# Performance work log

Hardware: AMD Instinct MI355X
Metric: run time of the kernel (lower is better)

The kernel has to match this reference:

```python
import jax, jax.numpy as jnp
import numpy as np

WS = 7          # window size
NH = 12         # num heads
DIM = 384       # embed dim
HD = DIM // NH  # head dim
BW = 2048       # B_ = batch * num_windows
N = WS * WS     # tokens per window


def _relative_position_index(ws):
    coords = np.stack(np.meshgrid(np.arange(ws), np.arange(ws), indexing='ij'))  # [2,ws,ws]
    cf = coords.reshape(2, -1)                      # [2, ws*ws]
    rel = cf[:, :, None] - cf[:, None, :]           # [2, N, N]
    rel = rel.transpose(1, 2, 0).copy()             # [N, N, 2]
    rel[:, :, 0] += ws - 1
    rel[:, :, 1] += ws - 1
    rel[:, :, 0] *= 2 * ws - 1
    return jnp.asarray(rel.sum(-1))                 # [N, N] int


REL_IDX = _relative_position_index(WS)


def setup_inputs() -> dict:
    key = jax.random.key(0)
    ks = jax.random.split(key, 6)
    return {
        'x': jax.random.normal(ks[0], (BW, N, DIM), dtype=jnp.float32),
        'qkv_w': jax.random.normal(ks[1], (3 * DIM, DIM), dtype=jnp.float32) * 0.02,
        'qkv_b': jax.random.normal(ks[2], (3 * DIM,), dtype=jnp.float32) * 0.02,
        'proj_w': jax.random.normal(ks[3], (DIM, DIM), dtype=jnp.float32) * 0.02,
        'proj_b': jax.random.normal(ks[4], (DIM,), dtype=jnp.float32) * 0.02,
        'rel_bias_table': jax.random.normal(ks[5], ((2 * WS - 1) ** 2, NH), dtype=jnp.float32) * 0.02,
    }


def reference(x, qkv_w, qkv_b, proj_w, proj_b, rel_bias_table):
    B_, n, c = x.shape
    scale = HD ** -0.5
    qkv = x @ qkv_w.T + qkv_b                                   # [B_, N, 3*DIM]
    qkv = qkv.reshape(B_, n, 3, NH, HD).transpose(2, 0, 3, 1, 4)  # [3, B_, H, N, HD]
    q, k, v = qkv[0], qkv[1], qkv[2]
    attn = jnp.einsum('bhnd,bhmd->bhnm', q * scale, k)           # [B_, H, N, N]
    bias = rel_bias_table[REL_IDX.reshape(-1)].reshape(n, n, NH)  # gather -> [N, N, H]
    attn = attn + bias.transpose(2, 0, 1)[None]                   # add [1, H, N, N]
    attn = jax.nn.softmax(attn, axis=-1)
    out = jnp.einsum('bhnm,bhmd->bhnd', attn, v)                 # [B_, H, N, HD]
    out = out.transpose(0, 2, 1, 3).reshape(B_, n, c)            # [B_, N, C]
    return out @ proj_w.T + proj_b
```

## Files before the change

### kernel.cpp

```cpp
#include <hip/hip_runtime.h>
#include <hip/hip_bf16.h>

#define NH 12
constexpr float SCALE = 0.17677669529663687f;
constexpr int TOKENS = 100352;

using f32x4  = __attribute__((ext_vector_type(4))) float;
using bf16x8 = __attribute__((ext_vector_type(8))) __bf16;

__device__ inline void gload_lds16(const void* g, void* l) {
  __builtin_amdgcn_global_load_lds(
      (const __attribute__((address_space(1))) void*)g,
      (__attribute__((address_space(3))) void*)l, 16, 0, 0);
}

__global__ __launch_bounds__(256) void wa_prep(
    const float* __restrict__ qkv_w, const float* __restrict__ proj_w,
    const float* __restrict__ tbl,
    __bf16* __restrict__ qkv_w_bf, __bf16* __restrict__ proj_w_bf,
    float* __restrict__ biasTt) {
  int p = blockIdx.x * 256 + threadIdx.x;
  if (p < 442368) { qkv_w_bf[p] = (__bf16)qkv_w[p]; return; }
  p -= 442368;
  if (p < 147456) { proj_w_bf[p] = (__bf16)proj_w[p]; return; }
  p -= 147456;
  if (p >= 49152) return;
  int h = p >> 12, rem = p & 4095, j = rem >> 6, i = rem & 63;
  float v;
  if (j >= 49) v = -1e30f;
  else if (i >= 49) v = 0.0f;
  else {
    int py = i / 7, px = i % 7, qy = j / 7, qx = j % 7;
    v = tbl[((py - qy + 6) * 13 + (px - qx + 6)) * NH + h];
  }
  biasTt[p] = v;
}

__global__ __launch_bounds__(256, 2) void wa_qkv(
    const float* __restrict__ x, const __bf16* __restrict__ wq,
    const float* __restrict__ qkv_b, __bf16* __restrict__ qkv) {
  __shared__ __bf16 As[64 * 384];
  __shared__ __bf16 Bs[2][128 * 64];
  const int t = threadIdx.x, lane = t & 63, wv = t >> 6;
  const int lr = lane & 15, ls = lane >> 4;
  const int mb = blockIdx.x;
  const int wr = wv >> 1, wc = wv & 1;
  #pragma unroll
  for (int i = 0; i < 12; ++i) {
    int p = i * 256 + t;
    int row = p / 48, slot = p - row * 48;
    const float* src = x + (size_t)(mb * 64 + row) * 384 + slot * 8;
    float4 a = *(const float4*)src;
    float4 b = *(const float4*)(src + 4);
    bf16x8 o;
    o[0] = (__bf16)a.x; o[1] = (__bf16)a.y; o[2] = (__bf16)a.z; o[3] = (__bf16)a.w;
    o[4] = (__bf16)b.x; o[5] = (__bf16)b.y; o[6] = (__bf16)b.z; o[7] = (__bf16)b.w;
    int sw = (slot & ~7) | ((slot & 7) ^ (row & 7));
    *(bf16x8*)(As + row * 384 + sw * 8) = o;
  }
  auto stage_b = [&](int st, int bp) {
    int nb = st / 6, kk = st - nb * 6;
    #pragma unroll
    for (int j = 0; j < 4; ++j) {
      int p = wv * 256 + j * 64 + lane;
      int c = p >> 3, sl = p & 7;
      int s = sl ^ (c & 7);
      gload_lds16(wq + (size_t)(nb * 128 + c) * 384 + kk * 64 + s * 8, Bs[bp] + p * 8);
    }
  };
  stage_b(0, 0);
  __syncthreads();
  for (int nb = 0; nb < 9; ++nb) {
    f32x4 acc[2][4] = {};
    for (int kk = 0; kk < 6; ++kk) {
      int st = nb * 6 + kk;
      if (st < 53) stage_b(st + 1, (st + 1) & 1);
      const __bf16* B = Bs[st & 1];
      #pragma unroll
      for (int ks = 0; ks < 2; ++ks) {
        bf16x8 af[2], bfr[4];
        #pragma unroll
        for (int rt = 0; rt < 2; ++rt) {
          int row = wr * 32 + rt * 16 + lr;
          int slot = kk * 8 + ks * 4 + ls;
          int sw = (slot & ~7) | ((slot & 7) ^ (row & 7));
          af[rt] = *(const bf16x8*)(As + row * 384 + sw * 8);
        }
        #pragma unroll
        for (int ct = 0; ct < 4; ++ct) {
          int c = wc * 64 + ct * 16 + lr;
          bfr[ct] = *(const bf16x8*)(B + (c * 8 + ((ks * 4 + ls) ^ (c & 7))) * 8);
        }
        #pragma unroll
        for (int rt = 0; rt < 2; ++rt)
          #pragma unroll
          for (int ct = 0; ct < 4; ++ct)
            acc[rt][ct] = __builtin_amdgcn_mfma_f32_16x16x32_bf16(af[rt], bfr[ct], acc[rt][ct], 0, 0, 0);
      }
      __syncthreads();
    }
    float bias[4];
    #pragma unroll
    for (int ct = 0; ct < 4; ++ct) bias[ct] = qkv_b[nb * 128 + wc * 64 + ct * 16 + lr];
    #pragma unroll
    for (int rt = 0; rt < 2; ++rt)
      #pragma unroll
      for (int r = 0; r < 4; ++r) {
        int row = wr * 32 + rt * 16 + ls * 4 + r;
        __bf16* dst = qkv + (size_t)(mb * 64 + row) * 1152 + nb * 128 + wc * 64;
        #pragma unroll
        for (int ct = 0; ct < 4; ++ct)
          dst[ct * 16 + lr] = (__bf16)(acc[rt][ct][r] + bias[ct]);
      }
  }
}

__global__ __launch_bounds__(256, 3) void wa_attn(
    const float* __restrict__ biasTt, __bf16* __restrict__ qkv) {
  __shared__ __bf16 Pbuf[4][4096];
  __shared__ __bf16 Vbuf[4][2048];
  const int t = threadIdx.x, lane = t & 63, wv = t >> 6;
  const int lr = lane & 15, ls = lane >> 4;
  const int pair = blockIdx.x * 4 + wv;
  const int w = pair / NH, h = pair - w * NH;
  const int w49 = w * 49;
  __bf16* Pw = Pbuf[wv];
  __bf16* Vw = Vbuf[wv];
  f32x4 zero = {0.f, 0.f, 0.f, 0.f};
  bf16x8 ones;
  #pragma unroll
  for (int e = 0; e < 8; ++e) ones[e] = (__bf16)1.0f;

  {
    int row = lane;
    int tok = w49 + (row < 49 ? row : 48);
    const bf16x8* vsrc = (const bf16x8*)(qkv + (size_t)tok * 1152 + 768 + h * 32);
    int f = (row & 3) ^ ((row >> 3) & 3);
    #pragma unroll
    for (int c = 0; c < 4; ++c)
      *(bf16x8*)(Vw + row * 32 + ((c ^ f) * 8)) = vsrc[c];
  }
  bf16x8 qa[4], kb[4];
  #pragma unroll
  for (int rt = 0; rt < 4; ++rt) {
    int tok = min(w49 + rt * 16 + lr, TOKENS - 1);
    qa[rt] = *(const bf16x8*)(qkv + (size_t)tok * 1152 + h * 32 + ls * 8);
  }
  #pragma unroll
  for (int ct = 0; ct < 4; ++ct) {
    int tok = min(w49 + ct * 16 + lr, TOKENS - 1);
    kb[ct] = *(const bf16x8*)(qkv + (size_t)tok * 1152 + 384 + h * 32 + ls * 8);
  }
  f32x4 sacc[4][4];
  #pragma unroll
  for (int rt = 0; rt < 4; ++rt)
    #pragma unroll
    for (int ct = 0; ct < 4; ++ct)
      sacc[rt][ct] = __builtin_amdgcn_mfma_f32_16x16x32_bf16(qa[rt], kb[ct], zero, 0, 0, 0);
  #pragma unroll
  for (int rt = 0; rt < 4; ++rt) {
    int row0 = rt * 16 + ls * 4;
    #pragma unroll
    for (int ct = 0; ct < 4; ++ct) {
      int col = ct * 16 + lr;
      float4 bias = *(const float4*)(biasTt + (size_t)(h * 64 + col) * 64 + row0);
      #pragma unroll
      for (int r = 0; r < 4; ++r) {
        int row = row0 + r;
        float pr = __expf(fmaf(sacc[rt][ct][r], SCALE, ((const float*)&bias)[r]));
        Pw[row * 64 + (((col >> 3) ^ (row & 7)) * 8) + (col & 7)] = (__bf16)pr;
      }
    }
  }
  f32x4 oacc[4][2] = {};
  f32x4 osum[4] = {zero, zero, zero, zero};
  #pragma unroll
  for (int ks = 0; ks < 2; ++ks) {
    bf16x8 vb0, vb1;
    #pragma unroll
    for (int e = 0; e < 8; ++e) {
      int j = ks * 32 + ls * 8 + e;
      int a = j * 32 + (((lr >> 3) ^ (e & 3) ^ ls) * 8) + (lr & 7);
      vb0[e] = Vw[a];
      vb1[e] = Vw[a ^ 16];
    }
    #pragma unroll
    for (int rt = 0; rt < 4; ++rt) {
      int row = rt * 16 + lr;
      bf16x8 pa = *(const bf16x8*)(Pw + row * 64 + (((ks * 4 + ls) ^ (row & 7)) * 8));
      oacc[rt][0] = __builtin_amdgcn_mfma_f32_16x16x32_bf16(pa, vb0, oacc[rt][0], 0, 0, 0);
      oacc[rt][1] = __builtin_amdgcn_mfma_f32_16x16x32_bf16(pa, vb1, oacc[rt][1], 0, 0, 0);
      osum[rt]    = __builtin_amdgcn_mfma_f32_16x16x32_bf16(pa, ones, osum[rt], 0, 0, 0);
    }
  }
  #pragma unroll
  for (int rt = 0; rt < 4; ++rt)
    #pragma unroll
    for (int r = 0; r < 4; ++r) {
      int row = rt * 16 + ls * 4 + r;
      if (row < 49) {
        float inv = 1.0f / osum[rt][r];
        __bf16* o = qkv + (size_t)(w49 + row) * 1152 + h * 32;
        o[lr]      = (__bf16)(oacc[rt][0][r] * inv);
        o[16 + lr] = (__bf16)(oacc[rt][1][r] * inv);
      }
    }
}

__global__ __launch_bounds__(256, 2) void wa_proj(
    const __bf16* __restrict__ qkv, const __bf16* __restrict__ pw,
    const float* __restrict__ proj_b, float* __restrict__ out) {
  __shared__ __bf16 As[64 * 384];
  __shared__ __bf16 Bs[2][128 * 64];
  const int t = threadIdx.x, lane = t & 63, wv = t >> 6;
  const int lr = lane & 15, ls = lane >> 4;
  const int mb = blockIdx.x;
  const int wr = wv >> 1, wc = wv & 1;
  #pragma unroll
  for (int j = 0; j < 12; ++j) {
    int p = wv * 768 + j * 64 + lane;
    int row = p / 48, sl = p - row * 48;
    int s = (sl & ~7) | ((sl & 7) ^ (row & 7));
    gload_lds16(qkv + (size_t)(mb * 64 + row) * 1152 + s * 8, As + p * 8);
  }
  auto stage_b = [&](int st, int bp) {
    int nb = st / 6, kk = st - nb * 6;
    #pragma unroll
    for (int j = 0; j < 4; ++j) {
      int p = wv * 256 + j * 64 + lane;
      int c = p >> 3, sl = p & 7;
      int s = sl ^ (c & 7);
      gload_lds16(pw + (size_t)(nb * 128 + c) * 384 + kk * 64 + s * 8, Bs[bp] + p * 8);
    }
  };
  stage_b(0, 0);
  __syncthreads();
  for (int nb = 0; nb < 3; ++nb) {
    f32x4 acc[2][4] = {};
    for (int kk = 0; kk < 6; ++kk) {
      int st = nb * 6 + kk;
      if (st < 17) stage_b(st + 1, (st + 1) & 1);
      const __bf16* B = Bs[st & 1];
      #pragma unroll
      for (int ks = 0; ks < 2; ++ks) {
        bf16x8 af[2], bfr[4];
        #pragma unroll
        for (int rt = 0; rt < 2; ++rt) {
          int row = wr * 32 + rt * 16 + lr;
          int slot = kk * 8 + ks * 4 + ls;
          int sw = (slot & ~7) | ((slot & 7) ^ (row & 7));
          af[rt] = *(const bf16x8*)(As + row * 384 + sw * 8);
        }
        #pragma unroll
        for (int ct = 0; ct < 4; ++ct) {
          int c = wc * 64 + ct * 16 + lr;
          bfr[ct] = *(const bf16x8*)(B + (c * 8 + ((ks * 4 + ls) ^ (c & 7))) * 8);
        }
        #pragma unroll
        for (int rt = 0; rt < 2; ++rt)
          #pragma unroll
          for (int ct = 0; ct < 4; ++ct)
            acc[rt][ct] = __builtin_amdgcn_mfma_f32_16x16x32_bf16(af[rt], bfr[ct], acc[rt][ct], 0, 0, 0);
      }
      __syncthreads();
    }
    #pragma unroll
    for (int ct = 0; ct < 4; ++ct) {
      int col = nb * 128 + wc * 64 + ct * 16 + lr;
      float b = proj_b[col];
      #pragma unroll
      for (int rt = 0; rt < 2; ++rt)
        #pragma unroll
        for (int r = 0; r < 4; ++r) {
          int row = wr * 32 + rt * 16 + ls * 4 + r;
          out[(size_t)(mb * 64 + row) * 384 + col] = acc[rt][ct][r] + b;
        }
    }
  }
}

extern "C" void kernel_launch(void* const* d_in, const int* in_sizes, int n_in,
                              void* d_out, int out_size, void* d_ws, size_t ws_size,
                              hipStream_t stream) {
  const float* x      = (const float*)d_in[0];
  const float* qkv_w  = (const float*)d_in[1];
  const float* qkv_b  = (const float*)d_in[2];
  const float* proj_w = (const float*)d_in[3];
  const float* proj_b = (const float*)d_in[4];
  const float* tbl    = (const float*)d_in[5];
  float* out = (float*)d_out;

  char* ws = (char*)d_ws;
  __bf16* qkv_w_bf  = (__bf16*)ws;
  __bf16* proj_w_bf = (__bf16*)(ws + 884736);
  float*  biasTt    = (float*)(ws + 1179648);
  __bf16* qkv_buf   = (__bf16*)(ws + 1376256);

  wa_prep<<<2496, 256, 0, stream>>>(qkv_w, proj_w, tbl, qkv_w_bf, proj_w_bf, biasTt);
  wa_qkv<<<1568, 256, 0, stream>>>(x, qkv_w_bf, qkv_b, qkv_buf);
  wa_attn<<<6144, 256, 0, stream>>>(biasTt, qkv_buf);
  wa_proj<<<1568, 256, 0, stream>>>(qkv_buf, proj_w_bf, proj_b, out);
}
```

Measured before the change: 389.1 us.

## Retile QKV GEMM to 128x128 output tiles with XCD-aware block mapping

The QKV projection kernel now has each block compute one 128x128 output tile instead of looping over all nine column blocks for 64 rows. Both A (x converted to bf16) and B are double-buffered over K, with the next x slice prefetched into registers during the MFMAs. Blocks are mapped so that the nine column blocks of one row block fall on the same XCD, which should let them share x in L2. Output is staged through LDS for coalesced 16-byte stores. In exchange, x is read and converted nine times per row block instead of once.

```diff
diff --git a/kernel.cpp b/kernel.cpp
--- a/kernel.cpp
+++ b/kernel.cpp
@@ -12,6 +12,13 @@
   __builtin_amdgcn_global_load_lds(
       (const __attribute__((address_space(1))) void*)g,
       (__attribute__((address_space(3))) void*)l, 16, 0, 0);
+}
+
+__device__ inline bf16x8 cvt8(float4 a, float4 b) {
+  bf16x8 o;
+  o[0] = (__bf16)a.x; o[1] = (__bf16)a.y; o[2] = (__bf16)a.z; o[3] = (__bf16)a.w;
+  o[4] = (__bf16)b.x; o[5] = (__bf16)b.y; o[6] = (__bf16)b.z; o[7] = (__bf16)b.w;
+  return o;
 }
 
 __global__ __launch_bounds__(256) void wa_prep(
@@ -36,82 +43,98 @@
   biasTt[p] = v;
 }
 
-__global__ __launch_bounds__(256, 2) void wa_qkv(
+__global__ __launch_bounds__(256, 2) void wa_qkv128(
     const float* __restrict__ x, const __bf16* __restrict__ wq,
     const float* __restrict__ qkv_b, __bf16* __restrict__ qkv) {
-  __shared__ __bf16 As[64 * 384];
-  __shared__ __bf16 Bs[2][128 * 64];
+  __shared__ __bf16 As[2][8192];
+  __shared__ __bf16 Bs[2][8192];
   const int t = threadIdx.x, lane = t & 63, wv = t >> 6;
   const int lr = lane & 15, ls = lane >> 4;
-  const int mb = blockIdx.x;
+  const int bid = blockIdx.x;
+  const int xcd = bid & 7, kb = bid >> 3;
+  const int mb = xcd * 98 + kb / 9, nb = kb - (kb / 9) * 9;
   const int wr = wv >> 1, wc = wv & 1;
-  #pragma unroll
-  for (int i = 0; i < 12; ++i) {
-    int p = i * 256 + t;
-    int row = p / 48, slot = p - row * 48;
-    const float* src = x + (size_t)(mb * 64 + row) * 384 + slot * 8;
-    float4 a = *(const float4*)src;
-    float4 b = *(const float4*)(src + 4);
-    bf16x8 o;
-    o[0] = (__bf16)a.x; o[1] = (__bf16)a.y; o[2] = (__bf16)a.z; o[3] = (__bf16)a.w;
-    o[4] = (__bf16)b.x; o[5] = (__bf16)b.y; o[6] = (__bf16)b.z; o[7] = (__bf16)b.w;
-    int sw = (slot & ~7) | ((slot & 7) ^ (row & 7));
-    *(bf16x8*)(As + row * 384 + sw * 8) = o;
-  }
-  auto stage_b = [&](int st, int bp) {
-    int nb = st / 6, kk = st - nb * 6;
-    #pragma unroll
-    for (int j = 0; j < 4; ++j) {
-      int p = wv * 256 + j * 64 + lane;
-      int c = p >> 3, sl = p & 7;
-      int s = sl ^ (c & 7);
-      gload_lds16(wq + (size_t)(nb * 128 + c) * 384 + kk * 64 + s * 8, Bs[bp] + p * 8);
-    }
-  };
-  stage_b(0, 0);
+  int crow[4], cs[4];
+  #pragma unroll
+  for (int j = 0; j < 4; ++j) {
+    int c = j * 256 + t;
+    crow[j] = c >> 3;
+    cs[j] = (c & 7) ^ ((c >> 3) & 7);
+  }
+  f32x4 acc[4][4] = {};
+  float4 av[4][2];
+  #pragma unroll
+  for (int j = 0; j < 4; ++j) {
+    const float* src = x + (size_t)(mb * 128 + crow[j]) * 384 + cs[j] * 8;
+    av[j][0] = *(const float4*)src;
+    av[j][1] = *(const float4*)(src + 4);
+    gload_lds16(wq + (size_t)(nb * 128 + crow[j]) * 384 + cs[j] * 8,
+                Bs[0] + (j * 256 + t) * 8);
+  }
+  #pragma unroll
+  for (int j = 0; j < 4; ++j)
+    *(bf16x8*)(As[0] + (size_t)(j * 256 + t) * 8) = cvt8(av[j][0], av[j][1]);
   __syncthreads();
-  for (int nb = 0; nb < 9; ++nb) {
-    f32x4 acc[2][4] = {};
-    for (int kk = 0; kk < 6; ++kk) {
-      int st = nb * 6 + kk;
-      if (st < 53) stage_b(st + 1, (st + 1) & 1);
-      const __bf16* B = Bs[st & 1];
-      #pragma unroll
-      for (int ks = 0; ks < 2; ++ks) {
-        bf16x8 af[2], bfr[4];
-        #pragma unroll
-        for (int rt = 0; rt < 2; ++rt) {
-          int row = wr * 32 + rt * 16 + lr;
-          int slot = kk * 8 + ks * 4 + ls;
-          int sw = (slot & ~7) | ((slot & 7) ^ (row & 7));
-          af[rt] = *(const bf16x8*)(As + row * 384 + sw * 8);
-        }
-        #pragma unroll
-        for (int ct = 0; ct < 4; ++ct) {
-          int c = wc * 64 + ct * 16 + lr;
-          bfr[ct] = *(const bf16x8*)(B + (c * 8 + ((ks * 4 + ls) ^ (c & 7))) * 8);
-        }
-        #pragma unroll
-        for (int rt = 0; rt < 2; ++rt)
-          #pragma unroll
-          for (int ct = 0; ct < 4; ++ct)
-            acc[rt][ct] = __builtin_amdgcn_mfma_f32_16x16x32_bf16(af[rt], bfr[ct], acc[rt][ct], 0, 0, 0);
-      }
-      __syncthreads();
-    }
-    float bias[4];
-    #pragma unroll
-    for (int ct = 0; ct < 4; ++ct) bias[ct] = qkv_b[nb * 128 + wc * 64 + ct * 16 + lr];
-    #pragma unroll
-    for (int rt = 0; rt < 2; ++rt)
-      #pragma unroll
-      for (int r = 0; r < 4; ++r) {
-        int row = wr * 32 + rt * 16 + ls * 4 + r;
-        __bf16* dst = qkv + (size_t)(mb * 64 + row) * 1152 + nb * 128 + wc * 64;
+  for (int kk = 0; kk < 6; ++kk) {
+    const int bp = kk & 1;
+    if (kk < 5) {
+      #pragma unroll
+      for (int j = 0; j < 4; ++j) {
+        const float* src = x + (size_t)(mb * 128 + crow[j]) * 384 + (kk + 1) * 64 + cs[j] * 8;
+        av[j][0] = *(const float4*)src;
+        av[j][1] = *(const float4*)(src + 4);
+        gload_lds16(wq + (size_t)(nb * 128 + crow[j]) * 384 + (kk + 1) * 64 + cs[j] * 8,
+                    Bs[bp ^ 1] + (j * 256 + t) * 8);
+      }
+    }
+    const __bf16* A = As[bp];
+    const __bf16* B = Bs[bp];
+    #pragma unroll
+    for (int ks = 0; ks < 2; ++ks) {
+      bf16x8 af[4], bfr[4];
+      #pragma unroll
+      for (int rt = 0; rt < 4; ++rt) {
+        int row = wr * 64 + rt * 16 + lr;
+        af[rt] = *(const bf16x8*)(A + row * 64 + (((ks * 4 + ls) ^ (row & 7)) * 8));
+      }
+      #pragma unroll
+      for (int ct = 0; ct < 4; ++ct) {
+        int c = wc * 64 + ct * 16 + lr;
+        bfr[ct] = *(const bf16x8*)(B + c * 64 + (((ks * 4 + ls) ^ (c & 7)) * 8));
+      }
+      #pragma unroll
+      for (int rt = 0; rt < 4; ++rt)
         #pragma unroll
         for (int ct = 0; ct < 4; ++ct)
-          dst[ct * 16 + lr] = (__bf16)(acc[rt][ct][r] + bias[ct]);
-      }
+          acc[rt][ct] = __builtin_amdgcn_mfma_f32_16x16x32_bf16(af[rt], bfr[ct], acc[rt][ct], 0, 0, 0);
+    }
+    if (kk < 5) {
+      #pragma unroll
+      for (int j = 0; j < 4; ++j)
+        *(bf16x8*)(As[bp ^ 1] + (size_t)(j * 256 + t) * 8) = cvt8(av[j][0], av[j][1]);
+    }
+    __syncthreads();
+  }
+  __bf16* Cs = (__bf16*)As;
+  float bias[4];
+  #pragma unroll
+  for (int ct = 0; ct < 4; ++ct) bias[ct] = qkv_b[nb * 128 + wc * 64 + ct * 16 + lr];
+  #pragma unroll
+  for (int rt = 0; rt < 4; ++rt)
+    #pragma unroll
+    for (int r = 0; r < 4; ++r) {
+      int row = wr * 64 + rt * 16 + ls * 4 + r;
+      #pragma unroll
+      for (int ct = 0; ct < 4; ++ct)
+        Cs[row * 128 + wc * 64 + ct * 16 + lr] = (__bf16)(acc[rt][ct][r] + bias[ct]);
+    }
+  __syncthreads();
+  #pragma unroll
+  for (int j = 0; j < 8; ++j) {
+    int c = j * 256 + t;
+    int row = c >> 4, q = c & 15;
+    *(bf16x8*)(qkv + (size_t)(mb * 128 + row) * 1152 + nb * 128 + q * 8) =
+        *(const bf16x8*)(Cs + c * 8);
   }
 }
 
@@ -297,7 +320,7 @@
   __bf16* qkv_buf   = (__bf16*)(ws + 1376256);
 
   wa_prep<<<2496, 256, 0, stream>>>(qkv_w, proj_w, tbl, qkv_w_bf, proj_w_bf, biasTt);
-  wa_qkv<<<1568, 256, 0, stream>>>(x, qkv_w_bf, qkv_b, qkv_buf);
+  wa_qkv128<<<7056, 256, 0, stream>>>(x, qkv_w_bf, qkv_b, qkv_buf);
   wa_attn<<<6144, 256, 0, stream>>>(biasTt, qkv_buf);
   wa_proj<<<1568, 256, 0, stream>>>(qkv_buf, proj_w_bf, proj_b, out);
 }
```

Measured after the change: 406.3 us. 4.4% more time.

## Split QKV and proj GEMMs into per-output-tile blocks with smaller LDS

Applied to the files above, without the earlier changes.

The QKV and projection GEMMs now launch one block per (64-row, 128-column) output tile instead of one block looping over all column tiles, with blocks grouped so eight row tiles share a weight column tile. LDS shrinks to a single 64-wide K slice per operand, which allows higher occupancy (launch bounds raised to 4). QKV output is staged through LDS for 16-byte coalesced stores. In exchange, x is re-read and re-converted from fp32 once per column tile (9x for QKV), and the double-buffered prefetch is dropped, so loads are no longer overlapped with MFMA work.

```diff
diff --git a/kernel.cpp b/kernel.cpp
--- a/kernel.cpp
+++ b/kernel.cpp
@@ -13,6 +13,15 @@
       (const __attribute__((address_space(1))) void*)g,
       (__attribute__((address_space(3))) void*)l, 16, 0, 0);
 }
+
+__device__ inline bf16x8 cvt8(float4 a, float4 b) {
+  bf16x8 o;
+  o[0] = (__bf16)a.x; o[1] = (__bf16)a.y; o[2] = (__bf16)a.z; o[3] = (__bf16)a.w;
+  o[4] = (__bf16)b.x; o[5] = (__bf16)b.y; o[6] = (__bf16)b.z; o[7] = (__bf16)b.w;
+  return o;
+}
+
+#define MFMA(a, b, c) __builtin_amdgcn_mfma_f32_16x16x32_bf16(a, b, c, 0, 0, 0)
 
 __global__ __launch_bounds__(256) void wa_prep(
     const float* __restrict__ qkv_w, const float* __restrict__ proj_w,
@@ -36,82 +45,82 @@
   biasTt[p] = v;
 }
 
-__global__ __launch_bounds__(256, 2) void wa_qkv(
+__global__ __launch_bounds__(256, 4) void wa_qkv(
     const float* __restrict__ x, const __bf16* __restrict__ wq,
     const float* __restrict__ qkv_b, __bf16* __restrict__ qkv) {
-  __shared__ __bf16 As[64 * 384];
-  __shared__ __bf16 Bs[2][128 * 64];
+  __shared__ __bf16 As[64 * 64];
+  __shared__ __bf16 Bs[128 * 64];
+  __shared__ __bf16 Cs[64 * 128];
   const int t = threadIdx.x, lane = t & 63, wv = t >> 6;
   const int lr = lane & 15, ls = lane >> 4;
-  const int mb = blockIdx.x;
+  const int bid = blockIdx.x;
+  const int q = bid / 72, rem = bid - q * 72;
+  const int nb = rem >> 3, mb = q * 8 + (rem & 7);
   const int wr = wv >> 1, wc = wv & 1;
-  #pragma unroll
-  for (int i = 0; i < 12; ++i) {
-    int p = i * 256 + t;
-    int row = p / 48, slot = p - row * 48;
-    const float* src = x + (size_t)(mb * 64 + row) * 384 + slot * 8;
-    float4 a = *(const float4*)src;
-    float4 b = *(const float4*)(src + 4);
-    bf16x8 o;
-    o[0] = (__bf16)a.x; o[1] = (__bf16)a.y; o[2] = (__bf16)a.z; o[3] = (__bf16)a.w;
-    o[4] = (__bf16)b.x; o[5] = (__bf16)b.y; o[6] = (__bf16)b.z; o[7] = (__bf16)b.w;
-    int sw = (slot & ~7) | ((slot & 7) ^ (row & 7));
-    *(bf16x8*)(As + row * 384 + sw * 8) = o;
-  }
-  auto stage_b = [&](int st, int bp) {
-    int nb = st / 6, kk = st - nb * 6;
+  f32x4 acc[2][4] = {};
+  for (int kk = 0; kk < 6; ++kk) {
+    if (kk) __syncthreads();
+    float4 a0[2], a1[2];
+    int rowA[2], cA[2];
+    #pragma unroll
+    for (int j = 0; j < 2; ++j) {
+      int p = j * 256 + t;
+      rowA[j] = p >> 3; cA[j] = p & 7;
+      const float* src = x + (size_t)(mb * 64 + rowA[j]) * 384 + kk * 64 + cA[j] * 8;
+      a0[j] = *(const float4*)src;
+      a1[j] = *(const float4*)(src + 4);
+    }
     #pragma unroll
     for (int j = 0; j < 4; ++j) {
-      int p = wv * 256 + j * 64 + lane;
+      int p = j * 256 + t;
       int c = p >> 3, sl = p & 7;
-      int s = sl ^ (c & 7);
-      gload_lds16(wq + (size_t)(nb * 128 + c) * 384 + kk * 64 + s * 8, Bs[bp] + p * 8);
-    }
-  };
-  stage_b(0, 0);
-  __syncthreads();
-  for (int nb = 0; nb < 9; ++nb) {
-    f32x4 acc[2][4] = {};
-    for (int kk = 0; kk < 6; ++kk) {
-      int st = nb * 6 + kk;
-      if (st < 53) stage_b(st + 1, (st + 1) & 1);
-      const __bf16* B = Bs[st & 1];
-      #pragma unroll
-      for (int ks = 0; ks < 2; ++ks) {
-        bf16x8 af[2], bfr[4];
+      gload_lds16(wq + (size_t)(nb * 128 + c) * 384 + kk * 64 + (sl ^ (c & 7)) * 8,
+                  Bs + p * 8);
+    }
+    #pragma unroll
+    for (int j = 0; j < 2; ++j) {
+      int cw = cA[j] ^ (rowA[j] & 7);
+      *(bf16x8*)(As + rowA[j] * 64 + cw * 8) = cvt8(a0[j], a1[j]);
+    }
+    __syncthreads();
+    #pragma unroll
+    for (int ks = 0; ks < 2; ++ks) {
+      bf16x8 af[2], bfr[4];
+      #pragma unroll
+      for (int rt = 0; rt < 2; ++rt) {
+        int row = wr * 32 + rt * 16 + lr;
+        af[rt] = *(const bf16x8*)(As + row * 64 + (((ks * 4 + ls) ^ (row & 7)) * 8));
+      }
+      #pragma unroll
+      for (int ct = 0; ct < 4; ++ct) {
+        int c = wc * 64 + ct * 16 + lr;
+        bfr[ct] = *(const bf16x8*)(Bs + c * 64 + (((ks * 4 + ls) ^ (c & 7)) * 8));
+      }
+      #pragma unroll
+      for (int rt = 0; rt < 2; ++rt)
         #pragma unroll
-        for (int rt = 0; rt < 2; ++rt) {
-          int row = wr * 32 + rt * 16 + lr;
-          int slot = kk * 8 + ks * 4 + ls;
-          int sw = (slot & ~7) | ((slot & 7) ^ (row & 7));
-          af[rt] = *(const bf16x8*)(As + row * 384 + sw * 8);
-        }
-        #pragma unroll
-        for (int ct = 0; ct < 4; ++ct) {
-          int c = wc * 64 + ct * 16 + lr;
-          bfr[ct] = *(const bf16x8*)(B + (c * 8 + ((ks * 4 + ls) ^ (c & 7))) * 8);
-        }
-        #pragma unroll
-        for (int rt = 0; rt < 2; ++rt)
-          #pragma unroll
-          for (int ct = 0; ct < 4; ++ct)
-            acc[rt][ct] = __builtin_amdgcn_mfma_f32_16x16x32_bf16(af[rt], bfr[ct], acc[rt][ct], 0, 0, 0);
-      }
-      __syncthreads();
-    }
-    float bias[4];
-    #pragma unroll
-    for (int ct = 0; ct < 4; ++ct) bias[ct] = qkv_b[nb * 128 + wc * 64 + ct * 16 + lr];
+        for (int ct = 0; ct < 4; ++ct)
+          acc[rt][ct] = MFMA(af[rt], bfr[ct], acc[rt][ct]);
+    }
+  }
+  #pragma unroll
+  for (int ct = 0; ct < 4; ++ct) {
+    float b = qkv_b[nb * 128 + wc * 64 + ct * 16 + lr];
     #pragma unroll
     for (int rt = 0; rt < 2; ++rt)
       #pragma unroll
       for (int r = 0; r < 4; ++r) {
         int row = wr * 32 + rt * 16 + ls * 4 + r;
-        __bf16* dst = qkv + (size_t)(mb * 64 + row) * 1152 + nb * 128 + wc * 64;
-        #pragma unroll
-        for (int ct = 0; ct < 4; ++ct)
-          dst[ct * 16 + lr] = (__bf16)(acc[rt][ct][r] + bias[ct]);
-      }
+        Cs[row * 128 + wc * 64 + ct * 16 + lr] = (__bf16)(acc[rt][ct][r] + b);
+      }
+  }
+  __syncthreads();
+  #pragma unroll
+  for (int j = 0; j < 4; ++j) {
+    int p = j * 256 + t;
+    int row = p >> 4, sub = p & 15;
+    *(bf16x8*)(qkv + (size_t)(mb * 64 + row) * 1152 + nb * 128 + sub * 8) =
+        *(const bf16x8*)(Cs + p * 8);
   }
 }
 
@@ -156,7 +165,7 @@
   for (int rt = 0; rt < 4; ++rt)
     #pragma unroll
     for (int ct = 0; ct < 4; ++ct)
-      sacc[rt][ct] = __builtin_amdgcn_mfma_f32_16x16x32_bf16(qa[rt], kb[ct], zero, 0, 0, 0);
+      sacc[rt][ct] = MFMA(qa[rt], kb[ct], zero);
   #pragma unroll
   for (int rt = 0; rt < 4; ++rt) {
     int row0 = rt * 16 + ls * 4;
@@ -188,9 +197,9 @@
     for (int rt = 0; rt < 4; ++rt) {
       int row = rt * 16 + lr;
       bf16x8 pa = *(const bf16x8*)(Pw + row * 64 + (((ks * 4 + ls) ^ (row & 7)) * 8));
-      oacc[rt][0] = __builtin_amdgcn_mfma_f32_16x16x32_bf16(pa, vb0, oacc[rt][0], 0, 0, 0);
-      oacc[rt][1] = __builtin_amdgcn_mfma_f32_16x16x32_bf16(pa, vb1, oacc[rt][1], 0, 0, 0);
-      osum[rt]    = __builtin_amdgcn_mfma_f32_16x16x32_bf16(pa, ones, osum[rt], 0, 0, 0);
+      oacc[rt][0] = MFMA(pa, vb0, oacc[rt][0]);
+      oacc[rt][1] = MFMA(pa, vb1, oacc[rt][1]);
+      osum[rt]    = MFMA(pa, ones, osum[rt]);
     }
   }
   #pragma unroll
@@ -207,75 +216,66 @@
     }
 }
 
-__global__ __launch_bounds__(256, 2) void wa_proj(
+__global__ __launch_bounds__(256, 4) void wa_proj(
     const __bf16* __restrict__ qkv, const __bf16* __restrict__ pw,
     const float* __restrict__ proj_b, float* __restrict__ out) {
-  __shared__ __bf16 As[64 * 384];
-  __shared__ __bf16 Bs[2][128 * 64];
+  __shared__ __bf16 As[64 * 64];
+  __shared__ __bf16 Bs[128 * 64];
   const int t = threadIdx.x, lane = t & 63, wv = t >> 6;
   const int lr = lane & 15, ls = lane >> 4;
-  const int mb = blockIdx.x;
+  const int bid = blockIdx.x;
+  const int q = bid / 24, rem = bid - q * 24;
+  const int nb = rem >> 3, mb = q * 8 + (rem & 7);
   const int wr = wv >> 1, wc = wv & 1;
-  #pragma unroll
-  for (int j = 0; j < 12; ++j) {
-    int p = wv * 768 + j * 64 + lane;
-    int row = p / 48, sl = p - row * 48;
-    int s = (sl & ~7) | ((sl & 7) ^ (row & 7));
-    gload_lds16(qkv + (size_t)(mb * 64 + row) * 1152 + s * 8, As + p * 8);
-  }
-  auto stage_b = [&](int st, int bp) {
-    int nb = st / 6, kk = st - nb * 6;
+  f32x4 acc[2][4] = {};
+  for (int kk = 0; kk < 6; ++kk) {
+    if (kk) __syncthreads();
+    #pragma unroll
+    for (int j = 0; j < 2; ++j) {
+      int p = j * 256 + t;
+      int row = p >> 3, sl = p & 7;
+      gload_lds16(qkv + (size_t)(mb * 64 + row) * 1152 + kk * 64 + (sl ^ (row & 7)) * 8,
+                  As + p * 8);
+    }
     #pragma unroll
     for (int j = 0; j < 4; ++j) {
-      int p = wv * 256 + j * 64 + lane;
+      int p = j * 256 + t;
       int c = p >> 3, sl = p & 7;
-      int s = sl ^ (c & 7);
-      gload_lds16(pw + (size_t)(nb * 128 + c) * 384 + kk * 64 + s * 8, Bs[bp] + p * 8);
-    }
-  };
-  stage_b(0, 0);
-  __syncthreads();
-  for (int nb = 0; nb < 3; ++nb) {
-    f32x4 acc[2][4] = {};
-    for (int kk = 0; kk < 6; ++kk) {
-      int st = nb * 6 + kk;
-      if (st < 17) stage_b(st + 1, (st + 1) & 1);
-      const __bf16* B = Bs[st & 1];
-      #pragma unroll
-      for (int ks = 0; ks < 2; ++ks) {
-        bf16x8 af[2], bfr[4];
-        #pragma unroll
-        for (int rt = 0; rt < 2; ++rt) {
-          int row = wr * 32 + rt * 16 + lr;
-          int slot = kk * 8 + ks * 4 + ls;
-          int sw = (slot & ~7) | ((slot & 7) ^ (row & 7));
-          af[rt] = *(const bf16x8*)(As + row * 384 + sw * 8);
-        }
-        #pragma unroll
-        for (int ct = 0; ct < 4; ++ct) {
-          int c = wc * 64 + ct * 16 + lr;
-          bfr[ct] = *(const bf16x8*)(B + (c * 8 + ((ks * 4 + ls) ^ (c & 7))) * 8);
-        }
-        #pragma unroll
-        for (int rt = 0; rt < 2; ++rt)
-          #pragma unroll
-          for (int ct = 0; ct < 4; ++ct)
-            acc[rt][ct] = __builtin_amdgcn_mfma_f32_16x16x32_bf16(af[rt], bfr[ct], acc[rt][ct], 0, 0, 0);
-      }
-      __syncthreads();
-    }
-    #pragma unroll
-    for (int ct = 0; ct < 4; ++ct) {
-      int col = nb * 128 + wc * 64 + ct * 16 + lr;
-      float b = proj_b[col];
+      gload_lds16(pw + (size_t)(nb * 128 + c) * 384 + kk * 64 + (sl ^ (c & 7)) * 8,
+                  Bs + p * 8);
+    }
+    __syncthreads();
+    #pragma unroll
+    for (int ks = 0; ks < 2; ++ks) {
+      bf16x8 af[2], bfr[4];
+      #pragma unroll
+      for (int rt = 0; rt < 2; ++rt) {
+        int row = wr * 32 + rt * 16 + lr;
+        af[rt] = *(const bf16x8*)(As + row * 64 + (((ks * 4 + ls) ^ (row & 7)) * 8));
+      }
+      #pragma unroll
+      for (int ct = 0; ct < 4; ++ct) {
+        int c = wc * 64 + ct * 16 + lr;
+        bfr[ct] = *(const bf16x8*)(Bs + c * 64 + (((ks * 4 + ls) ^ (c & 7)) * 8));
+      }
       #pragma unroll
       for (int rt = 0; rt < 2; ++rt)
         #pragma unroll
-        for (int r = 0; r < 4; ++r) {
-          int row = wr * 32 + rt * 16 + ls * 4 + r;
-          out[(size_t)(mb * 64 + row) * 384 + col] = acc[rt][ct][r] + b;
-        }
-    }
+        for (int ct = 0; ct < 4; ++ct)
+          acc[rt][ct] = MFMA(af[rt], bfr[ct], acc[rt][ct]);
+    }
+  }
+  #pragma unroll
+  for (int ct = 0; ct < 4; ++ct) {
+    int col = nb * 128 + wc * 64 + ct * 16 + lr;
+    float b = proj_b[col];
+    #pragma unroll
+    for (int rt = 0; rt < 2; ++rt)
+      #pragma unroll
+      for (int r = 0; r < 4; ++r) {
+        int row = wr * 32 + rt * 16 + ls * 4 + r;
+        out[(size_t)(mb * 64 + row) * 384 + col] = acc[rt][ct][r] + b;
+      }
   }
 }
 
@@ -297,7 +297,7 @@
   __bf16* qkv_buf   = (__bf16*)(ws + 1376256);
 
   wa_prep<<<2496, 256, 0, stream>>>(qkv_w, proj_w, tbl, qkv_w_bf, proj_w_bf, biasTt);
-  wa_qkv<<<1568, 256, 0, stream>>>(x, qkv_w_bf, qkv_b, qkv_buf);
+  wa_qkv<<<14112, 256, 0, stream>>>(x, qkv_w_bf, qkv_b, qkv_buf);
   wa_attn<<<6144, 256, 0, stream>>>(biasTt, qkv_buf);
-  wa_proj<<<1568, 256, 0, stream>>>(qkv_buf, proj_w_bf, proj_b, out);
-}
+  wa_proj<<<4704, 256, 0, stream>>>(qkv_buf, proj_w_bf, proj_b, out);
+}
```

New measurement: 336.5 us. -13.5%, faster.
